# Kernel tuning notes

Hardware: AMD Instinct MI355X
Metric: run time of the kernel (lower is better)

Reference implementation:

```python
import jax, jax.numpy as jnp
import numpy as np
from jax import lax

T, B, D = 200, 1024, 128  # max_len, batch, units (= input feature dim)


def setup_inputs() -> dict:
    key = jax.random.key(0)
    ks = jax.random.split(key, 16)
    s = 1.0 / np.sqrt(D)
    inp = {
        "inputs": jax.random.normal(ks[0], (T, B, D), dtype=jnp.float32),
        "state": jnp.zeros((B, D), dtype=jnp.float32),
        "att_score": jax.random.uniform(ks[1], (T, B, 1), dtype=jnp.float32),
        # binary validity mask [B, T], float because it multiplies the state
        "mask": (jax.random.uniform(ks[2], (B, T)) < 0.9).astype(jnp.float32),
        "max_len": T,
        # u gate (Bilinear: Dense(a) with bias + Dense(b) no bias)
        "Wau": jax.random.normal(ks[3], (D, D), dtype=jnp.float32) * s,
        "bau": jnp.zeros((D,), dtype=jnp.float32),
        "Wbu": jax.random.normal(ks[4], (D, D), dtype=jnp.float32) * s,
        # r gate
        "War": jax.random.normal(ks[5], (D, D), dtype=jnp.float32) * s,
        "bar": jnp.zeros((D,), dtype=jnp.float32),
        "Wbr": jax.random.normal(ks[6], (D, D), dtype=jnp.float32) * s,
        # candidate memory
        "Wac": jax.random.normal(ks[7], (D, D), dtype=jnp.float32) * s,
        "bac": jnp.zeros((D,), dtype=jnp.float32),
        "Wbc": jax.random.normal(ks[8], (D, D), dtype=jnp.float32) * s,
    }
    return inp


def reference(inputs, state, att_score, mask, max_len,
              Wau, bau, Wbu, War, bar, Wbr, Wac, bac, Wbc):
    # time-major mask [T, B, 1]
    mask_t = jnp.swapaxes(mask, 0, 1)[:, :, None]

    def step(s, xs):
        x, a, m = xs  # x:[B,D], a:[B,1], m:[B,1]
        u = jax.nn.sigmoid(x @ Wau + bau + s @ Wbu)
        r = jax.nn.sigmoid(x @ War + bar + s @ Wbr)
        c = jnp.tanh(x @ Wac + bac + r * (s @ Wbc))
        u_ = a * u
        new = (1.0 - u_) * s + u_ * c
        s = new * m + s * (1.0 - m)
        return s, None

    final_state, _ = lax.scan(step, state, (inputs, att_score, mask_t))
    return final_state
```

## Files before the change

### kernel.cpp

```cpp
#include <hip/hip_runtime.h>
#include <stdint.h>

#define T_LEN 200
#define B_SZ  1024
#define D_DIM 128
#define LOG2E 1.44269504088896340736f

typedef __bf16 bf16_t;
typedef __bf16 bf16x8 __attribute__((ext_vector_type(8)));
typedef float  f32x4  __attribute__((ext_vector_type(4)));

union BF8 { bf16x8 v; bf16_t e[8]; };

__device__ inline uint32_t pk_bf16(float a, float b) {
  uint32_t ua = __float_as_uint(a), ub = __float_as_uint(b);
  ua += 0x7fffu + ((ua >> 16) & 1u);
  ub += 0x7fffu + ((ub >> 16) & 1u);
  return (ua >> 16) | (ub & 0xffff0000u);
}
__device__ inline float rcp_f(float x) { return __builtin_amdgcn_rcpf(x); }

#define BAR_LDS() asm volatile("s_waitcnt lgkmcnt(0)\n\ts_barrier" ::: "memory")

__global__ __launch_bounds__(512, 2) void augru_fused(
    const float* __restrict__ x,
    const float* __restrict__ state,
    const float* __restrict__ att,
    const float* __restrict__ mask,
    const float* __restrict__ Wau, const float* __restrict__ bau,
    const float* __restrict__ Wbu,
    const float* __restrict__ War, const float* __restrict__ bar,
    const float* __restrict__ Wbr,
    const float* __restrict__ Wac, const float* __restrict__ bac,
    const float* __restrict__ Wbc,
    float* __restrict__ out)
{
  __shared__ bf16_t xb[2][2048];
  __shared__ bf16_t sb[2][2048];
  __shared__ float  am_lds[T_LEN * 16];

  const int tid = threadIdx.x;
  const int w  = tid >> 6;
  const int l  = tid & 63;
  const int lm = l & 15;
  const int lg = l >> 4;
  const int bb = blockIdx.x;
  const int R0 = bb * 16;
  const int col = w * 16 + lm;

  BF8 xu[4], xr[4], xc[4];
  BF8 su[4], sr[4], sc[4];
#pragma unroll
  for (int kk = 0; kk < 4; ++kk) {
#pragma unroll
    for (int j = 0; j < 8; ++j) {
      int k = kk * 32 + lg * 8 + j;
      xu[kk].e[j] = (bf16_t)(Wau[k * 128 + col] * LOG2E);
      xr[kk].e[j] = (bf16_t)(War[k * 128 + col] * LOG2E);
      xc[kk].e[j] = (bf16_t)(Wac[k * 128 + col] * (2.0f * LOG2E));
      su[kk].e[j] = (bf16_t)(Wbu[k * 128 + col] * LOG2E);
      sr[kk].e[j] = (bf16_t)(Wbr[k * 128 + col] * LOG2E);
      sc[kk].e[j] = (bf16_t)(Wbc[k * 128 + col] * (2.0f * LOG2E));
    }
  }
  const float b_u = bau[col] * LOG2E;
  const float b_r = bar[col] * LOG2E;
  const float b_c = bac[col] * (2.0f * LOG2E);

  for (int idx = tid; idx < T_LEN * 16; idx += 512) {
    int t = idx >> 4, row = idx & 15;
    am_lds[idx] = att[t * B_SZ + R0 + row] * mask[(R0 + row) * T_LEN + t];
  }

  float sreg[4];
#pragma unroll
  for (int i = 0; i < 4; ++i)
    sreg[i] = state[(R0 + lg * 4 + i) * 128 + col];

  for (int idx = tid; idx < 2048; idx += 512) {
    int row = idx >> 7, k = idx & 127;
    sb[0][(k >> 5) * 512 + ((k >> 3) & 3) * 128 + row * 8 + (k & 7)] =
        (bf16_t)state[(R0 + row) * 128 + k];
  }

  const int srow = tid & 15;
  const int sc4  = tid >> 4;
  const int stg_pos = (sc4 >> 3) * 512 + ((sc4 >> 1) & 3) * 128 + srow * 8
                    + (sc4 & 1) * 4;
  const float* xrow = x + (size_t)(R0 + srow) * 128 + sc4 * 4;
  const size_t xstep = (size_t)B_SZ * 128;

  {
    float4 v = *(const float4*)(xrow);
    uint2 p; p.x = pk_bf16(v.x, v.y); p.y = pk_bf16(v.z, v.w);
    *(uint2*)&xb[0][stg_pos] = p;
  }
  float4 xq0 = *(const float4*)(xrow + 1 * xstep);
  float4 xq1 = *(const float4*)(xrow + 2 * xstep);
  float4 xq2 = *(const float4*)(xrow + 3 * xstep);

  __syncthreads();

  auto step = [&](int t) {
    const int rp = t & 1;

    {
      uint2 p; p.x = pk_bf16(xq0.x, xq0.y); p.y = pk_bf16(xq0.z, xq0.w);
      *(uint2*)&xb[rp ^ 1][stg_pos] = p;
    }
    xq0 = xq1; xq1 = xq2;
    int tl = t + 4; if (tl > T_LEN - 1) tl = T_LEN - 1;
    xq2 = *(const float4*)(xrow + (size_t)tl * xstep);

    bf16x8 ax[4], as_[4];
#pragma unroll
    for (int kk = 0; kk < 4; ++kk) {
      ax[kk]  = *(const bf16x8*)&xb[rp][kk * 512 + 8 * l];
      as_[kk] = *(const bf16x8*)&sb[rp][kk * 512 + 8 * l];
    }

    f32x4 aU = {b_u, b_u, b_u, b_u};
    f32x4 aR = {b_r, b_r, b_r, b_r};
    f32x4 aC = {b_c, b_c, b_c, b_c};
    f32x4 bU = {0.f, 0.f, 0.f, 0.f};
    f32x4 bR = {0.f, 0.f, 0.f, 0.f};
    f32x4 bC = {0.f, 0.f, 0.f, 0.f};
#pragma unroll
    for (int kk = 0; kk < 4; ++kk) {
      aU = __builtin_amdgcn_mfma_f32_16x16x32_bf16(ax[kk],  xu[kk].v, aU, 0, 0, 0);
      bU = __builtin_amdgcn_mfma_f32_16x16x32_bf16(as_[kk], su[kk].v, bU, 0, 0, 0);
      aR = __builtin_amdgcn_mfma_f32_16x16x32_bf16(ax[kk],  xr[kk].v, aR, 0, 0, 0);
      bR = __builtin_amdgcn_mfma_f32_16x16x32_bf16(as_[kk], sr[kk].v, bR, 0, 0, 0);
      aC = __builtin_amdgcn_mfma_f32_16x16x32_bf16(ax[kk],  xc[kk].v, aC, 0, 0, 0);
      bC = __builtin_amdgcn_mfma_f32_16x16x32_bf16(as_[kk], sc[kk].v, bC, 0, 0, 0);
    }

    union { float4 v; float e[4]; } amu;
    amu.v = *(const float4*)&am_lds[t * 16 + lg * 4];

    bf16_t* wbuf = sb[rp ^ 1];
    const int wbase = (col >> 5) * 512 + ((col >> 3) & 3) * 128 + lg * 32
                    + (col & 7);
#pragma unroll
    for (int i = 0; i < 4; ++i) {
      float zu = aU[i] + bU[i];
      float zr = aR[i] + bR[i];
      float u  = rcp_f(1.0f + __builtin_amdgcn_exp2f(-zu));
      float r  = rcp_f(1.0f + __builtin_amdgcn_exp2f(-zr));
      float wc = fmaf(r, bC[i], aC[i]);
      float cg = fmaf(-2.0f, rcp_f(__builtin_amdgcn_exp2f(wc) + 1.0f), 1.0f);
      float sf = fmaf(amu.e[i] * u, cg - sreg[i], sreg[i]);
      sreg[i] = sf;
      wbuf[wbase + 8 * i] = (bf16_t)sf;
    }

    BAR_LDS();
  };

#pragma unroll 1
  for (int t = 0; t < T_LEN; t += 2) {
    step(t);
    step(t + 1);
  }

#pragma unroll
  for (int i = 0; i < 4; ++i)
    out[(R0 + lg * 4 + i) * 128 + col] = sreg[i];
}

extern "C" void kernel_launch(void* const* d_in, const int* in_sizes, int n_in,
                              void* d_out, int out_size, void* d_ws, size_t ws_size,
                              hipStream_t stream)
{
  const float* x    = (const float*)d_in[0];
  const float* st   = (const float*)d_in[1];
  const float* att  = (const float*)d_in[2];
  const float* mask = (const float*)d_in[3];
  const float* Wau  = (const float*)d_in[5];
  const float* bau  = (const float*)d_in[6];
  const float* Wbu  = (const float*)d_in[7];
  const float* War  = (const float*)d_in[8];
  const float* bar  = (const float*)d_in[9];
  const float* Wbr  = (const float*)d_in[10];
  const float* Wac  = (const float*)d_in[11];
  const float* bac  = (const float*)d_in[12];
  const float* Wbc  = (const float*)d_in[13];

  (void)d_ws; (void)ws_size;

  augru_fused<<<dim3(64), dim3(512), 0, stream>>>(
      x, st, att, mask, Wau, bau, Wbu, War, bar, Wbr, Wac, bac, Wbc,
      (float*)d_out);
}
```

Measured before the change: 313.7 us.

## Precompute next-step input projections and swizzle state LDS layout

```diff
diff --git a/kernel.cpp b/kernel.cpp
--- a/kernel.cpp
+++ b/kernel.cpp
@@ -79,80 +79,102 @@
 
   for (int idx = tid; idx < 2048; idx += 512) {
     int row = idx >> 7, k = idx & 127;
-    sb[0][(k >> 5) * 512 + ((k >> 3) & 3) * 128 + row * 8 + (k & 7)] =
+    sb[0][(k >> 3) * 128 + (row ^ (2 * ((k >> 3) & 1))) * 8 + (k & 7)] =
         (bf16_t)state[(R0 + row) * 128 + k];
   }
 
   const int srow = tid & 15;
   const int sc4  = tid >> 4;
-  const int stg_pos = (sc4 >> 3) * 512 + ((sc4 >> 1) & 3) * 128 + srow * 8
-                    + (sc4 & 1) * 4;
+  const int stg_pos = (sc4 >> 1) * 128 + srow * 8 + (sc4 & 1) * 4;
   const float* xrow = x + (size_t)(R0 + srow) * 128 + sc4 * 4;
   const size_t xstep = (size_t)B_SZ * 128;
 
   {
-    float4 v = *(const float4*)(xrow);
-    uint2 p; p.x = pk_bf16(v.x, v.y); p.y = pk_bf16(v.z, v.w);
-    *(uint2*)&xb[0][stg_pos] = p;
-  }
-  float4 xq0 = *(const float4*)(xrow + 1 * xstep);
-  float4 xq1 = *(const float4*)(xrow + 2 * xstep);
-  float4 xq2 = *(const float4*)(xrow + 3 * xstep);
+    float4 v0 = *(const float4*)(xrow);
+    float4 v1 = *(const float4*)(xrow + xstep);
+    uint2 p0; p0.x = pk_bf16(v0.x, v0.y); p0.y = pk_bf16(v0.z, v0.w);
+    uint2 p1; p1.x = pk_bf16(v1.x, v1.y); p1.y = pk_bf16(v1.z, v1.w);
+    *(uint2*)&xb[0][stg_pos] = p0;
+    *(uint2*)&xb[1][stg_pos] = p1;
+  }
+  float4 xq0 = *(const float4*)(xrow + 2 * xstep);
+  float4 xq1 = *(const float4*)(xrow + 3 * xstep);
+  float4 xq2 = *(const float4*)(xrow + 4 * xstep);
 
   __syncthreads();
+
+  f32x4 gU = {b_u, b_u, b_u, b_u};
+  f32x4 gR = {b_r, b_r, b_r, b_r};
+  f32x4 gC = {b_c, b_c, b_c, b_c};
+  {
+    bf16x8 ax[4];
+#pragma unroll
+    for (int kk = 0; kk < 4; ++kk)
+      ax[kk] = *(const bf16x8*)&xb[0][kk * 512 + 8 * l];
+#pragma unroll
+    for (int kk = 0; kk < 4; ++kk) {
+      gU = __builtin_amdgcn_mfma_f32_16x16x32_bf16(ax[kk], xu[kk].v, gU, 0, 0, 0);
+      gR = __builtin_amdgcn_mfma_f32_16x16x32_bf16(ax[kk], xr[kk].v, gR, 0, 0, 0);
+      gC = __builtin_amdgcn_mfma_f32_16x16x32_bf16(ax[kk], xc[kk].v, gC, 0, 0, 0);
+    }
+  }
+  union F4 { float4 v; float e[4]; } amv;
+  amv.v = *(const float4*)&am_lds[lg * 4];
+
+  const int lx8   = 8 * (l ^ (2 * (lg & 1)));
+  const int psi   = 2 * ((col >> 3) & 1);
+  const int wbase = (col >> 3) * 128 + lg * 32 + (col & 7);
+
+  BAR_LDS();
 
   auto step = [&](int t) {
     const int rp = t & 1;
 
     {
       uint2 p; p.x = pk_bf16(xq0.x, xq0.y); p.y = pk_bf16(xq0.z, xq0.w);
-      *(uint2*)&xb[rp ^ 1][stg_pos] = p;
+      *(uint2*)&xb[rp][stg_pos] = p;
     }
     xq0 = xq1; xq1 = xq2;
-    int tl = t + 4; if (tl > T_LEN - 1) tl = T_LEN - 1;
+    int tl = t + 5; if (tl > T_LEN - 1) tl = T_LEN - 1;
     xq2 = *(const float4*)(xrow + (size_t)tl * xstep);
 
     bf16x8 ax[4], as_[4];
 #pragma unroll
     for (int kk = 0; kk < 4; ++kk) {
-      ax[kk]  = *(const bf16x8*)&xb[rp][kk * 512 + 8 * l];
-      as_[kk] = *(const bf16x8*)&sb[rp][kk * 512 + 8 * l];
-    }
-
-    f32x4 aU = {b_u, b_u, b_u, b_u};
-    f32x4 aR = {b_r, b_r, b_r, b_r};
-    f32x4 aC = {b_c, b_c, b_c, b_c};
-    f32x4 bU = {0.f, 0.f, 0.f, 0.f};
-    f32x4 bR = {0.f, 0.f, 0.f, 0.f};
+      ax[kk]  = *(const bf16x8*)&xb[rp ^ 1][kk * 512 + 8 * l];
+      as_[kk] = *(const bf16x8*)&sb[rp][kk * 512 + lx8];
+    }
+
+    f32x4 aU = gU, aR = gR;
     f32x4 bC = {0.f, 0.f, 0.f, 0.f};
+    f32x4 nU = {b_u, b_u, b_u, b_u};
+    f32x4 nR = {b_r, b_r, b_r, b_r};
+    f32x4 nC = {b_c, b_c, b_c, b_c};
 #pragma unroll
     for (int kk = 0; kk < 4; ++kk) {
-      aU = __builtin_amdgcn_mfma_f32_16x16x32_bf16(ax[kk],  xu[kk].v, aU, 0, 0, 0);
-      bU = __builtin_amdgcn_mfma_f32_16x16x32_bf16(as_[kk], su[kk].v, bU, 0, 0, 0);
-      aR = __builtin_amdgcn_mfma_f32_16x16x32_bf16(ax[kk],  xr[kk].v, aR, 0, 0, 0);
-      bR = __builtin_amdgcn_mfma_f32_16x16x32_bf16(as_[kk], sr[kk].v, bR, 0, 0, 0);
-      aC = __builtin_amdgcn_mfma_f32_16x16x32_bf16(ax[kk],  xc[kk].v, aC, 0, 0, 0);
+      aU = __builtin_amdgcn_mfma_f32_16x16x32_bf16(as_[kk], su[kk].v, aU, 0, 0, 0);
+      nU = __builtin_amdgcn_mfma_f32_16x16x32_bf16(ax[kk],  xu[kk].v, nU, 0, 0, 0);
+      aR = __builtin_amdgcn_mfma_f32_16x16x32_bf16(as_[kk], sr[kk].v, aR, 0, 0, 0);
+      nR = __builtin_amdgcn_mfma_f32_16x16x32_bf16(ax[kk],  xr[kk].v, nR, 0, 0, 0);
       bC = __builtin_amdgcn_mfma_f32_16x16x32_bf16(as_[kk], sc[kk].v, bC, 0, 0, 0);
-    }
-
-    union { float4 v; float e[4]; } amu;
-    amu.v = *(const float4*)&am_lds[t * 16 + lg * 4];
+      nC = __builtin_amdgcn_mfma_f32_16x16x32_bf16(ax[kk],  xc[kk].v, nC, 0, 0, 0);
+    }
 
     bf16_t* wbuf = sb[rp ^ 1];
-    const int wbase = (col >> 5) * 512 + ((col >> 3) & 3) * 128 + lg * 32
-                    + (col & 7);
 #pragma unroll
     for (int i = 0; i < 4; ++i) {
-      float zu = aU[i] + bU[i];
-      float zr = aR[i] + bR[i];
-      float u  = rcp_f(1.0f + __builtin_amdgcn_exp2f(-zu));
-      float r  = rcp_f(1.0f + __builtin_amdgcn_exp2f(-zr));
-      float wc = fmaf(r, bC[i], aC[i]);
+      float u  = rcp_f(1.0f + __builtin_amdgcn_exp2f(-aU[i]));
+      float r  = rcp_f(1.0f + __builtin_amdgcn_exp2f(-aR[i]));
+      float wc = fmaf(r, bC[i], gC[i]);
       float cg = fmaf(-2.0f, rcp_f(__builtin_amdgcn_exp2f(wc) + 1.0f), 1.0f);
-      float sf = fmaf(amu.e[i] * u, cg - sreg[i], sreg[i]);
+      float sf = fmaf(amv.e[i] * u, cg - sreg[i], sreg[i]);
       sreg[i] = sf;
-      wbuf[wbase + 8 * i] = (bf16_t)sf;
-    }
+      wbuf[wbase + 8 * (i ^ psi)] = (bf16_t)sf;
+    }
+
+    gU = nU; gR = nR; gC = nC;
+    int ta = t + 1; if (ta > T_LEN - 1) ta = T_LEN - 1;
+    amv.v = *(const float4*)&am_lds[ta * 16 + lg * 4];
 
     BAR_LDS();
   };
```

New measurement: 309.2 us. No clear change (-1.4%).
